# Optimization experiments

Hardware: AMD Instinct MI355X
Metric: run time of the kernel (lower is better)

Reference implementation:

```python
import jax, jax.numpy as jnp
import numpy as np


def setup_inputs() -> dict:
    key = jax.random.key(0)
    k1, k2 = jax.random.split(key)
    B, C, H, W = 32, 256, 32, 32
    K = 2048
    x = jax.random.normal(k1, (B, C, H, W), dtype=jnp.float32)
    # nn.Embedding init in source is uniform(-1/K, 1/K); use normal scaled similarly-small
    embed_w = jax.random.uniform(k2, (K, C), dtype=jnp.float32, minval=-1.0 / K, maxval=1.0 / K)
    return {"x": x, "embed_w": embed_w}


def reference(x, embed_w):
    # x: [B, C, H, W] -> tokens [B, HW, C]
    B, C, H, W = x.shape
    tokens = jnp.transpose(x, (0, 2, 3, 1)).reshape(B, H * W, C)
    # Euclidean argmin: argmin_k ||t - e_k||^2 = argmin_k (||e_k||^2 - 2 t.e_k)
    # Avoids materializing sqrt cdist; argmin is identical.
    e_sq = jnp.sum(embed_w * embed_w, axis=-1)           # [K]
    dots = jnp.einsum('bnc,kc->bnk', tokens, embed_w)    # [B, HW, K] dominant intermediate
    embed_idx = jnp.argmin(e_sq[None, None, :] - 2.0 * dots, axis=-1)  # [B, HW]
    # one-hot matmul in source == gather
    quantized = embed_w[embed_idx]                        # [B, HW, C]
    quantize = jnp.transpose(quantized.reshape(B, H, W, C), (0, 3, 1, 2))  # [B, C, H, W]
    embed_index = embed_idx.reshape(B, H, W)
    loss = jnp.zeros((1,), dtype=jnp.float32)  # eval path: loss stays 0
    return quantize, embed_index, loss
```

## Files before the change

kernel.cpp:

```cpp
#include <hip/hip_runtime.h>


#define CDIM 256
#define KDIM 2048
#define HW   1024
#define NTOK 32768
#define QOFF 8388608
#define LOFF (QOFF + NTOK)

typedef _Float16 f16x8 __attribute__((ext_vector_type(8)));
typedef float    f32x4 __attribute__((ext_vector_type(4)));

__device__ __forceinline__ f16x8 ld16(const char* p) { return *(const f16x8*)(p); }

__global__ __launch_bounds__(256) void prep_kernel(const float* __restrict__ x,
                                                   const float* __restrict__ ew,
                                                   char* __restrict__ Aws,
                                                   char* __restrict__ Ews,
                                                   float* __restrict__ esq,
                                                   float* __restrict__ out) {
    __shared__ float tile[32][257];
    const int t = threadIdx.x;
    if (blockIdx.x < 1024) {
        const int bid = blockIdx.x;
        const int b = bid >> 5;
        const int kc = (bid >> 2) & 7;
        const int c0 = kc * 32;
        const int hw0 = (bid & 3) * 256;
        #pragma unroll 8
        for (int r = 0; r < 32; ++r)
            tile[r][t] = x[((size_t)(b * CDIM + c0 + r) << 10) + hw0 + t];
        __syncthreads();
        union { _Float16 h[32]; uint4 q[4]; } Hb, Lb;
        #pragma unroll 8
        for (int r = 0; r < 32; ++r) {
            const float xs = tile[r][t] * 64.0f;
            const _Float16 hh = (_Float16)xs;
            Hb.h[r] = hh;
            Lb.h[r] = (_Float16)(xs - (float)hh);
        }
        const int tok = b * HW + hw0 + t;
        const int p = tok >> 6, row = tok & 63;
        char* d = Aws + (size_t)p * 65536 + kc * 8192 + row * 16;
        #pragma unroll
        for (int g = 0; g < 4; ++g) {
            *(uint4*)(d + g * 1024)        = Hb.q[g];
            *(uint4*)(d + 4096 + g * 1024) = Lb.q[g];
        }
    } else {
        const int bid = blockIdx.x - 1024;
        const int code = bid * 8 + (t >> 5);
        const int u = t & 31;
        const float4 v0 = *(const float4*)&ew[(size_t)code * CDIM + u * 8];
        const float4 v1 = *(const float4*)&ew[(size_t)code * CDIM + u * 8 + 4];
        float s = v0.x*v0.x + v0.y*v0.y + v0.z*v0.z + v0.w*v0.w
                + v1.x*v1.x + v1.y*v1.y + v1.z*v1.z + v1.w*v1.w;
        #pragma unroll
        for (int m = 16; m >= 1; m >>= 1) s += __shfl_xor(s, m, 32);
        if (u == 0) esq[code] = s * 2097152.0f;
        const float e[8] = {v0.x, v0.y, v0.z, v0.w, v1.x, v1.y, v1.z, v1.w};
        union { _Float16 h[8]; uint4 q; } H, L;
        #pragma unroll
        for (int j = 0; j < 8; ++j) {
            const float ev = e[j] * 32768.0f;
            const _Float16 hh = (_Float16)ev;
            H.h[j] = hh;
            L.h[j] = (_Float16)(ev - (float)hh);
        }
        const int kc = u >> 2, g = u & 3;
        const int p = code >> 6, row = code & 63;
        char* d = Ews + (size_t)p * 65536 + kc * 8192 + g * 1024 + row * 16;
        *(uint4*)d = H.q;
        *(uint4*)(d + 4096) = L.q;
        if (bid == 0 && t == 0) out[LOFF] = 0.0f;
    }
}

__global__ __launch_bounds__(256, 3) void vqmm_kernel(const char* __restrict__ Aws,
                                                      const char* __restrict__ Ews,
                                                      const float* __restrict__ esq,
                                                      float* __restrict__ cv,
                                                      int* __restrict__ ci) {
    __shared__ __align__(16) char elds[32768];

    const int t = threadIdx.x;
    const int bid = blockIdx.x;
    const int by = (bid & 7) | ((bid >> 8) << 3);
    const int bx = (bid >> 3) & 31;
    const int lane = t & 63, w = t >> 6;
    const int g = lane >> 4, lr = lane & 15;
    const int r = (bid + w) & 1;

    const char* pa = Aws + (size_t)(by * 4 + w) * 65536 + g * 1024 + lr * 16;
    const char* esrc = Ews + (size_t)bx * 65536;

    f16x8 fa[4], fb[4], ec[4], ed[4];
    uint4 rg[4];

    #pragma unroll
    for (int j = 0; j < 4; ++j)
        rg[j] = *(const uint4*)(esrc + j * 4096 + t * 16);
    {
        const char* pa0 = pa + r * 8192;
        #pragma unroll
        for (int m = 0; m < 4; ++m) {
            fa[m] = ld16(pa0 + m * 256);
            fb[m] = ld16(pa0 + 4096 + m * 256);
        }
    }
    #pragma unroll
    for (int j = 0; j < 4; ++j)
        *(uint4*)(elds + j * 4096 + t * 16) = rg[j];
    __syncthreads();

    const f32x4 zf = {0.f, 0.f, 0.f, 0.f};
    f32x4 acc[4][4];
    #pragma unroll
    for (int m = 0; m < 4; ++m)
        #pragma unroll
        for (int n = 0; n < 4; ++n) acc[m][n] = zf;

    {
        const char* ep0 = elds + r * 8192 + g * 1024 + lr * 16;
        #pragma unroll
        for (int n = 0; n < 4; ++n) {
            ec[n] = ld16(ep0 + n * 256);
            ed[n] = ld16(ep0 + 4096 + n * 256);
        }
    }

    #pragma unroll
    for (int q = 0; q < 4; ++q) {
        const int buf = (q & 1) * 16384;
        if (q < 3) {
            const char* s2 = esrc + (q + 1) * 16384;
            #pragma unroll
            for (int j = 0; j < 4; ++j)
                rg[j] = *(const uint4*)(s2 + j * 4096 + t * 16);
        }
        if (q > 0) {
            const char* ep = elds + buf + r * 8192 + g * 1024 + lr * 16;
            #pragma unroll
            for (int n = 0; n < 4; ++n) {
                ec[n] = ld16(ep + n * 256);
                ed[n] = ld16(ep + 4096 + n * 256);
            }
        }
        #pragma unroll
        for (int p = 0; p < 2; ++p) {
            const bool lastPhase = (q == 3) && (p == 1);
            const int kcA = (p == 0) ? (2 * q + (r ^ 1)) : (2 * (q + 1) + r);
            const char* pan = pa + kcA * 8192;
            #pragma unroll
            for (int m = 0; m < 4; ++m) {
                __builtin_amdgcn_s_setprio(1);
                #pragma unroll
                for (int n = 0; n < 4; ++n) {
                    acc[m][n] = __builtin_amdgcn_mfma_f32_16x16x32_f16(fa[m], ec[n], acc[m][n], 0, 0, 0);
                    acc[m][n] = __builtin_amdgcn_mfma_f32_16x16x32_f16(fa[m], ed[n], acc[m][n], 0, 0, 0);
                    acc[m][n] = __builtin_amdgcn_mfma_f32_16x16x32_f16(fb[m], ec[n], acc[m][n], 0, 0, 0);
                }
                __builtin_amdgcn_s_setprio(0);
                if (!lastPhase) {
                    fa[m] = ld16(pan + m * 256);
                    fb[m] = ld16(pan + 4096 + m * 256);
                }
            }
            if (p == 0) {
                const char* en = elds + buf + (r ^ 1) * 8192 + g * 1024 + lr * 16;
                #pragma unroll
                for (int n = 0; n < 4; ++n) {
                    ec[n] = ld16(en + n * 256);
                    ed[n] = ld16(en + 4096 + n * 256);
                }
            }
        }
        if (q < 3) {
            char* nb = elds + ((q + 1) & 1) * 16384;
            #pragma unroll
            for (int j = 0; j < 4; ++j)
                *(uint4*)(nb + j * 4096 + t * 16) = rg[j];
            __syncthreads();
        }
    }

    float eq[4];
    #pragma unroll
    for (int n = 0; n < 4; ++n) eq[n] = esq[bx * 64 + n * 16 + lr];
    #pragma unroll
    for (int m = 0; m < 4; ++m) {
        #pragma unroll
        for (int rr = 0; rr < 4; ++rr) {
            float bv = 3.4e38f; int bi = 0x7fffffff;
            #pragma unroll
            for (int n = 0; n < 4; ++n) {
                const float d = fmaf(-2.0f, acc[m][n][rr], eq[n]);
                const int cidx = bx * 64 + n * 16 + lr;
                if (d < bv) { bv = d; bi = cidx; }
            }
            #pragma unroll
            for (int mk = 1; mk < 16; mk <<= 1) {
                const float ov = __shfl_xor(bv, mk, 16);
                const int   oi = __shfl_xor(bi, mk, 16);
                if (ov < bv || (ov == bv && oi < bi)) { bv = ov; bi = oi; }
            }
            if (lr == 0) {
                const size_t o = (size_t)bx * NTOK + by * 256 + w * 64 + m * 16 + g * 4 + rr;
                cv[o] = bv; ci[o] = bi;
            }
        }
    }
}

__global__ __launch_bounds__(256) void merge_gather_kernel(const float* __restrict__ cv,
                                                           const int* __restrict__ ci,
                                                           const float* __restrict__ ew,
                                                           float* __restrict__ out) {
    __shared__ float redV[256];
    __shared__ int   redI[256];
    __shared__ int   sIdx[64];
    const int t = threadIdx.x;
    const int n0 = blockIdx.x * 64;
    {
        const int tok = n0 + (t & 63);
        const int s0 = (t >> 6) * 8;
        float bv = 3.4e38f; int bi = 0x7fffffff;
        #pragma unroll
        for (int s = 0; s < 8; ++s) {
            const float v  = cv[(size_t)(s0 + s) * NTOK + tok];
            const int   i2 = ci[(size_t)(s0 + s) * NTOK + tok];
            if (v < bv || (v == bv && i2 < bi)) { bv = v; bi = i2; }
        }
        redV[t] = bv; redI[t] = bi;
    }
    __syncthreads();
    if (t < 64) {
        float bv = redV[t]; int bi = redI[t];
        #pragma unroll
        for (int s = 1; s < 4; ++s) {
            const float v = redV[t + s * 64]; const int i2 = redI[t + s * 64];
            if (v < bv || (v == bv && i2 < bi)) { bv = v; bi = i2; }
        }
        sIdx[t] = bi;
        out[QOFF + n0 + t] = (float)bi;
    }
    __syncthreads();
    const int b = n0 >> 10, hw0 = n0 & (HW - 1);
    const int i = t & 63, cg = t >> 6;
    const int kidx = sIdx[i];
    const float* er = ew + (size_t)kidx * CDIM;
    float* ob = out + (size_t)b * CDIM * HW + hw0 + i;
    #pragma unroll
    for (int p = 0; p < CDIM / 4; ++p) {
        const int c = cg * 64 + p;
        ob[(size_t)c * HW] = er[c];
    }
}

extern "C" void kernel_launch(void* const* d_in, const int* in_sizes, int n_in,
                              void* d_out, int out_size, void* d_ws, size_t ws_size,
                              hipStream_t stream) {
    const float* x  = (const float*)d_in[0];
    const float* ew = (const float*)d_in[1];
    float* out = (float*)d_out;
    char* ws = (char*)d_ws;

    char*  Aws = ws;
    char*  Ews = ws + 33554432;
    float* esq = (float*)(ws + 35651584);
    float* cvv = (float*)(ws + 35659776);
    int*   cii = (int*)(ws + 39854080);

    prep_kernel<<<1280, 256, 0, stream>>>(x, ew, Aws, Ews, esq, out);
    vqmm_kernel<<<4096, 256, 0, stream>>>(Aws, Ews, esq, cvv, cii);
    merge_gather_kernel<<<NTOK / 64, 256, 0, stream>>>(cvv, cii, ew, out);
}
```

Baseline: 135.2 us.

## Triple-buffer codebook LDS tiles and split MFMA phases to overlap fragment reloads

The single LDS double buffer becomes a triple buffer (48KB). The global prefetch of the codebook tile is issued two stages ahead and the barrier is moved so LDS writes happen mid-iteration. Each MFMA phase is split into two halves (fa/fb×ec, then fa×ed), so the ec/ed and fa/fb fragment reloads can be issued earlier and hidden behind matrix work. The larger LDS footprint (48KB × 3 blocks per CU with launch bounds 3) may limit occupancy.

```diff
diff --git a/kernel.cpp b/kernel.cpp
--- a/kernel.cpp
+++ b/kernel.cpp
@@ -81,7 +81,7 @@
                                                       const float* __restrict__ esq,
                                                       float* __restrict__ cv,
                                                       int* __restrict__ ci) {
-    __shared__ __align__(16) char elds[32768];
+    __shared__ __align__(16) char elds[49152];
 
     const int t = threadIdx.x;
     const int bid = blockIdx.x;
@@ -93,6 +93,7 @@
 
     const char* pa = Aws + (size_t)(by * 4 + w) * 65536 + g * 1024 + lr * 16;
     const char* esrc = Ews + (size_t)bx * 65536;
+    const int eoff = g * 1024 + lr * 16;
 
     f16x8 fa[4], fb[4], ec[4], ed[4];
     uint4 rg[4];
@@ -111,6 +112,9 @@
     #pragma unroll
     for (int j = 0; j < 4; ++j)
         *(uint4*)(elds + j * 4096 + t * 16) = rg[j];
+    #pragma unroll
+    for (int j = 0; j < 4; ++j)
+        rg[j] = *(const uint4*)(esrc + 16384 + j * 4096 + t * 16);
     __syncthreads();
 
     const f32x4 zf = {0.f, 0.f, 0.f, 0.f};
@@ -121,7 +125,7 @@
         for (int n = 0; n < 4; ++n) acc[m][n] = zf;
 
     {
-        const char* ep0 = elds + r * 8192 + g * 1024 + lr * 16;
+        const char* ep0 = elds + r * 8192 + eoff;
         #pragma unroll
         for (int n = 0; n < 4; ++n) {
             ec[n] = ld16(ep0 + n * 256);
@@ -129,60 +133,59 @@
         }
     }
 
+#define VQ_PHASE(EN, PAN, LAST)                                                                  \
+    {                                                                                            \
+        _Pragma("unroll")                                                                        \
+        for (int m = 0; m < 4; ++m) {                                                            \
+            __builtin_amdgcn_s_setprio(1);                                                       \
+            _Pragma("unroll")                                                                    \
+            for (int n = 0; n < 4; ++n)                                                          \
+                acc[m][n] = __builtin_amdgcn_mfma_f32_16x16x32_f16(fa[m], ec[n], acc[m][n], 0, 0, 0); \
+            _Pragma("unroll")                                                                    \
+            for (int n = 0; n < 4; ++n)                                                          \
+                acc[m][n] = __builtin_amdgcn_mfma_f32_16x16x32_f16(fb[m], ec[n], acc[m][n], 0, 0, 0); \
+            __builtin_amdgcn_s_setprio(0);                                                       \
+            if (!(LAST)) fb[m] = ld16((PAN) + 4096 + m * 256);                                   \
+        }                                                                                        \
+        if (!(LAST)) {                                                                           \
+            _Pragma("unroll")                                                                    \
+            for (int n = 0; n < 4; ++n) ec[n] = ld16((EN) + n * 256);                            \
+        }                                                                                        \
+        _Pragma("unroll")                                                                        \
+        for (int m = 0; m < 4; ++m) {                                                            \
+            __builtin_amdgcn_s_setprio(1);                                                       \
+            _Pragma("unroll")                                                                    \
+            for (int n = 0; n < 4; ++n)                                                          \
+                acc[m][n] = __builtin_amdgcn_mfma_f32_16x16x32_f16(fa[m], ed[n], acc[m][n], 0, 0, 0); \
+            __builtin_amdgcn_s_setprio(0);                                                       \
+            if (!(LAST)) fa[m] = ld16((PAN) + m * 256);                                          \
+        }                                                                                        \
+        if (!(LAST)) {                                                                           \
+            _Pragma("unroll")                                                                    \
+            for (int n = 0; n < 4; ++n) ed[n] = ld16((EN) + 4096 + n * 256);                     \
+        }                                                                                        \
+    }
+
     #pragma unroll
     for (int q = 0; q < 4; ++q) {
-        const int buf = (q & 1) * 16384;
+        const int bufC = (q % 3) * 16384;
+        const int bufN = ((q + 1) % 3) * 16384;
+        VQ_PHASE(elds + bufC + (r ^ 1) * 8192 + eoff, pa + (2 * q + (r ^ 1)) * 8192, false)
         if (q < 3) {
-            const char* s2 = esrc + (q + 1) * 16384;
             #pragma unroll
             for (int j = 0; j < 4; ++j)
-                rg[j] = *(const uint4*)(s2 + j * 4096 + t * 16);
-        }
-        if (q > 0) {
-            const char* ep = elds + buf + r * 8192 + g * 1024 + lr * 16;
-            #pragma unroll
-            for (int n = 0; n < 4; ++n) {
-                ec[n] = ld16(ep + n * 256);
-                ed[n] = ld16(ep + 4096 + n * 256);
-            }
-        }
-        #pragma unroll
-        for (int p = 0; p < 2; ++p) {
-            const bool lastPhase = (q == 3) && (p == 1);
-            const int kcA = (p == 0) ? (2 * q + (r ^ 1)) : (2 * (q + 1) + r);
-            const char* pan = pa + kcA * 8192;
-            #pragma unroll
-            for (int m = 0; m < 4; ++m) {
-                __builtin_amdgcn_s_setprio(1);
+                *(uint4*)(elds + bufN + j * 4096 + t * 16) = rg[j];
+            __syncthreads();
+            if (q < 2) {
+                const char* s2 = esrc + (q + 2) * 16384;
                 #pragma unroll
-                for (int n = 0; n < 4; ++n) {
-                    acc[m][n] = __builtin_amdgcn_mfma_f32_16x16x32_f16(fa[m], ec[n], acc[m][n], 0, 0, 0);
-                    acc[m][n] = __builtin_amdgcn_mfma_f32_16x16x32_f16(fa[m], ed[n], acc[m][n], 0, 0, 0);
-                    acc[m][n] = __builtin_amdgcn_mfma_f32_16x16x32_f16(fb[m], ec[n], acc[m][n], 0, 0, 0);
-                }
-                __builtin_amdgcn_s_setprio(0);
-                if (!lastPhase) {
-                    fa[m] = ld16(pan + m * 256);
-                    fb[m] = ld16(pan + 4096 + m * 256);
-                }
-            }
-            if (p == 0) {
-                const char* en = elds + buf + (r ^ 1) * 8192 + g * 1024 + lr * 16;
-                #pragma unroll
-                for (int n = 0; n < 4; ++n) {
-                    ec[n] = ld16(en + n * 256);
-                    ed[n] = ld16(en + 4096 + n * 256);
-                }
-            }
-        }
-        if (q < 3) {
-            char* nb = elds + ((q + 1) & 1) * 16384;
-            #pragma unroll
-            for (int j = 0; j < 4; ++j)
-                *(uint4*)(nb + j * 4096 + t * 16) = rg[j];
-            __syncthreads();
-        }
-    }
+                for (int j = 0; j < 4; ++j)
+                    rg[j] = *(const uint4*)(s2 + j * 4096 + t * 16);
+            }
+        }
+        VQ_PHASE(elds + bufN + r * 8192 + eoff, pa + (2 * (q + 1) + r) * 8192, q == 3)
+    }
+#undef VQ_PHASE
 
     float eq[4];
     #pragma unroll
```

After: 151.9 us. +12.4%, slower.

## Drop LDS staging of codebook tiles; load fragments directly from global with rotated k-order

Applied to the files above, without the earlier changes.

Removes the shared-memory double buffer and barriers for the codebook tile. Each wave now loads its codebook fragments straight from global memory, relying on L1/L2 reuse across the block's four waves. The k-chunk order is rotated per block (bid&7) to spread cache traffic, and A-operand loads use nontemporal hints. This drops __syncthreads and LDS writes but adds redundant global/L2 traffic for the shared codebook fragments, and the register prefetch now has less latency slack.

```diff
diff --git a/kernel.cpp b/kernel.cpp
--- a/kernel.cpp
+++ b/kernel.cpp
@@ -12,6 +12,9 @@
 typedef float    f32x4 __attribute__((ext_vector_type(4)));
 
 __device__ __forceinline__ f16x8 ld16(const char* p) { return *(const f16x8*)(p); }
+__device__ __forceinline__ f16x8 ld16nt(const char* p) {
+    return __builtin_nontemporal_load((const f16x8*)(p));
+}
 
 __global__ __launch_bounds__(256) void prep_kernel(const float* __restrict__ x,
                                                    const float* __restrict__ ew,
@@ -81,37 +84,32 @@
                                                       const float* __restrict__ esq,
                                                       float* __restrict__ cv,
                                                       int* __restrict__ ci) {
-    __shared__ __align__(16) char elds[32768];
-
     const int t = threadIdx.x;
     const int bid = blockIdx.x;
     const int by = (bid & 7) | ((bid >> 8) << 3);
     const int bx = (bid >> 3) & 31;
     const int lane = t & 63, w = t >> 6;
     const int g = lane >> 4, lr = lane & 15;
-    const int r = (bid + w) & 1;
+    const int kc0 = bid & 7;
 
     const char* pa = Aws + (size_t)(by * 4 + w) * 65536 + g * 1024 + lr * 16;
-    const char* esrc = Ews + (size_t)bx * 65536;
+    const char* pe = Ews + (size_t)bx * 65536 + g * 1024 + lr * 16;
 
     f16x8 fa[4], fb[4], ec[4], ed[4];
-    uint4 rg[4];
-
-    #pragma unroll
-    for (int j = 0; j < 4; ++j)
-        rg[j] = *(const uint4*)(esrc + j * 4096 + t * 16);
     {
-        const char* pa0 = pa + r * 8192;
+        const char* pa0 = pa + kc0 * 8192;
+        const char* pe0 = pe + kc0 * 8192;
         #pragma unroll
         for (int m = 0; m < 4; ++m) {
-            fa[m] = ld16(pa0 + m * 256);
-            fb[m] = ld16(pa0 + 4096 + m * 256);
-        }
-    }
-    #pragma unroll
-    for (int j = 0; j < 4; ++j)
-        *(uint4*)(elds + j * 4096 + t * 16) = rg[j];
-    __syncthreads();
+            fa[m] = ld16nt(pa0 + m * 256);
+            fb[m] = ld16nt(pa0 + 4096 + m * 256);
+        }
+        #pragma unroll
+        for (int n = 0; n < 4; ++n) {
+            ec[n] = ld16(pe0 + n * 256);
+            ed[n] = ld16(pe0 + 4096 + n * 256);
+        }
+    }
 
     const f32x4 zf = {0.f, 0.f, 0.f, 0.f};
     f32x4 acc[4][4];
@@ -120,67 +118,33 @@
         #pragma unroll
         for (int n = 0; n < 4; ++n) acc[m][n] = zf;
 
-    {
-        const char* ep0 = elds + r * 8192 + g * 1024 + lr * 16;
-        #pragma unroll
-        for (int n = 0; n < 4; ++n) {
-            ec[n] = ld16(ep0 + n * 256);
-            ed[n] = ld16(ep0 + 4096 + n * 256);
-        }
-    }
-
-    #pragma unroll
-    for (int q = 0; q < 4; ++q) {
-        const int buf = (q & 1) * 16384;
-        if (q < 3) {
-            const char* s2 = esrc + (q + 1) * 16384;
-            #pragma unroll
-            for (int j = 0; j < 4; ++j)
-                rg[j] = *(const uint4*)(s2 + j * 4096 + t * 16);
-        }
-        if (q > 0) {
-            const char* ep = elds + buf + r * 8192 + g * 1024 + lr * 16;
+    #pragma unroll
+    for (int i = 0; i < 8; ++i) {
+        const bool last = (i == 7);
+        const int kcn = (kc0 + i + 1) & 7;
+        const char* pan = pa + kcn * 8192;
+        #pragma unroll
+        for (int m = 0; m < 4; ++m) {
+            __builtin_amdgcn_s_setprio(1);
             #pragma unroll
             for (int n = 0; n < 4; ++n) {
-                ec[n] = ld16(ep + n * 256);
-                ed[n] = ld16(ep + 4096 + n * 256);
-            }
-        }
-        #pragma unroll
-        for (int p = 0; p < 2; ++p) {
-            const bool lastPhase = (q == 3) && (p == 1);
-            const int kcA = (p == 0) ? (2 * q + (r ^ 1)) : (2 * (q + 1) + r);
-            const char* pan = pa + kcA * 8192;
-            #pragma unroll
-            for (int m = 0; m < 4; ++m) {
-                __builtin_amdgcn_s_setprio(1);
-                #pragma unroll
-                for (int n = 0; n < 4; ++n) {
-                    acc[m][n] = __builtin_amdgcn_mfma_f32_16x16x32_f16(fa[m], ec[n], acc[m][n], 0, 0, 0);
-                    acc[m][n] = __builtin_amdgcn_mfma_f32_16x16x32_f16(fa[m], ed[n], acc[m][n], 0, 0, 0);
-                    acc[m][n] = __builtin_amdgcn_mfma_f32_16x16x32_f16(fb[m], ec[n], acc[m][n], 0, 0, 0);
-                }
-                __builtin_amdgcn_s_setprio(0);
-                if (!lastPhase) {
-                    fa[m] = ld16(pan + m * 256);
-                    fb[m] = ld16(pan + 4096 + m * 256);
-                }
-            }
-            if (p == 0) {
-                const char* en = elds + buf + (r ^ 1) * 8192 + g * 1024 + lr * 16;
-                #pragma unroll
-                for (int n = 0; n < 4; ++n) {
-                    ec[n] = ld16(en + n * 256);
-                    ed[n] = ld16(en + 4096 + n * 256);
-                }
-            }
-        }
-        if (q < 3) {
-            char* nb = elds + ((q + 1) & 1) * 16384;
-            #pragma unroll
-            for (int j = 0; j < 4; ++j)
-                *(uint4*)(nb + j * 4096 + t * 16) = rg[j];
-            __syncthreads();
+                acc[m][n] = __builtin_amdgcn_mfma_f32_16x16x32_f16(fa[m], ec[n], acc[m][n], 0, 0, 0);
+                acc[m][n] = __builtin_amdgcn_mfma_f32_16x16x32_f16(fa[m], ed[n], acc[m][n], 0, 0, 0);
+                acc[m][n] = __builtin_amdgcn_mfma_f32_16x16x32_f16(fb[m], ec[n], acc[m][n], 0, 0, 0);
+            }
+            __builtin_amdgcn_s_setprio(0);
+            if (!last) {
+                fa[m] = ld16nt(pan + m * 256);
+                fb[m] = ld16nt(pan + 4096 + m * 256);
+            }
+        }
+        if (!last) {
+            const char* pen = pe + kcn * 8192;
+            #pragma unroll
+            for (int n = 0; n < 4; ++n) {
+                ec[n] = ld16(pen + n * 256);
+                ed[n] = ld16(pen + 4096 + n * 256);
+            }
         }
     }
 
```

Result: slower. 144.8 us (+7.1%).
